# Kernel tuning notes

Hardware: AMD Instinct MI355X
Metric: run time of the kernel (lower is better)

## Reference

```python
import jax, jax.numpy as jnp
import numpy as np

BS, SEQ, NV, DM, K = 128, 2048, 64, 512, 64
MAX_ITER, TOL = 10, 1e-4


def setup_inputs() -> dict:
    key = jax.random.key(0)
    k1, k2, k3, k4 = jax.random.split(key, 4)
    x = jax.random.normal(k1, (BS, SEQ, NV), jnp.float32)
    bound = 1.0 / np.sqrt(SEQ)
    W = jax.random.uniform(k2, (DM, SEQ), jnp.float32, -bound, bound)  # nn.Linear weight
    b = jax.random.uniform(k3, (DM,), jnp.float32, -bound, bound)
    centroids = jax.random.normal(k4, (K, DM), jnp.float32)  # kaiming-uniform-init param (random stand-in)
    return {"x": x, "W": W, "b": b, "centroids": centroids}


def _kmeans(x_emb, centroids):
    # x_emb: [N, DM]; fixed-length scan with a `done` flag emulating torch's tol break.
    N = x_emb.shape[0]
    x_sq = jnp.sum(x_emb * x_emb, axis=1, keepdims=True)  # [N,1]

    def body(state, _):
        cent, ids, done = state
        # squared euclidean distances (argmin-equivalent to cdist p=2)
        d2 = x_sq - 2.0 * (x_emb @ cent.T) + jnp.sum(cent * cent, axis=1)  # [N,K]
        new_ids = jnp.argmin(d2, axis=1)
        sums = jax.ops.segment_sum(x_emb, new_ids, num_segments=K)          # [K,DM]
        counts = jax.ops.segment_sum(jnp.ones((N,), x_emb.dtype), new_ids, num_segments=K)
        means = sums / jnp.maximum(counts, 1.0)[:, None]
        new_cent = jnp.where((counts > 0)[:, None], means, cent)  # empty cluster keeps old centroid
        shift = jnp.linalg.norm(new_cent - cent)
        cent_out = jnp.where(done, cent, new_cent)
        ids_out = jnp.where(done, ids, new_ids)
        done_out = done | (shift < TOL)
        return (cent_out, ids_out, done_out), None

    init = (centroids, jnp.zeros((N,), jnp.int32), jnp.array(False))
    (cent, ids, _), _ = jax.lax.scan(body, init, None, length=MAX_ITER)
    return ids, cent


def reference(x, W, b, centroids):
    # x: [bs, seq, n_vars] -> permute -> linear(seq->d_model) -> [bs*n_vars, d_model]
    xt = jnp.transpose(x, (0, 2, 1))                 # [bs, n_vars, seq]
    x_emb = (xt @ W.T + b).reshape(-1, DM)           # [bs*n_vars, d_model]
    ids, cent = _kmeans(x_emb, centroids)
    prob = jax.nn.one_hot(ids, K, dtype=jnp.float32).reshape(BS, NV, K)
    return prob, cent, x_emb
```

## Files before the change

### kernel.cpp

```cpp
#include <hip/hip_runtime.h>

#define SEQ 2048
#define NVAR 64
#define DMODEL 512
#define BSZ 128
#define KC 64
#define NPT (BSZ*NVAR)
#define MAXIT 10

typedef __bf16 bf16x8 __attribute__((ext_vector_type(8)));
typedef float f32x4 __attribute__((ext_vector_type(4)));

__device__ __forceinline__ void load_lds16(const void* g, void* l) {
  __builtin_amdgcn_global_load_lds((const __attribute__((address_space(1))) void*)g,
                                   (__attribute__((address_space(3))) void*)l, 16, 0, 0);
}

__device__ __forceinline__ unsigned short bf16_rn(float x) {
  unsigned int u = __float_as_uint(x);
  u += 0x7fffu + ((u >> 16) & 1u);
  return (unsigned short)(u >> 16);
}

__global__ __launch_bounds__(256) void init_k(const float* __restrict__ c0,
    float* __restrict__ cent, unsigned short* __restrict__ centh,
    unsigned short* __restrict__ centl, float* __restrict__ csq4,
    int* __restrict__ done, float* __restrict__ shift2, int* __restrict__ ticket) {
  const int k = blockIdx.x, t = threadIdx.x;
  __shared__ float red[256];
  float v0, v1;
  {
    int d = t;
    v0 = c0[k * DMODEL + d];
    cent[k * DMODEL + d] = v0;
    unsigned short h = bf16_rn(v0);
    centh[k * DMODEL + d] = h;
    centl[k * DMODEL + d] = bf16_rn(v0 - __uint_as_float((unsigned)h << 16));
  }
  {
    int d = t + 256;
    v1 = c0[k * DMODEL + d];
    cent[k * DMODEL + d] = v1;
    unsigned short h = bf16_rn(v1);
    centh[k * DMODEL + d] = h;
    centl[k * DMODEL + d] = bf16_rn(v1 - __uint_as_float((unsigned)h << 16));
  }
  red[t] = v0 * v0; __syncthreads();
  for (int s = 64; s > 0; s >>= 1) { if ((t & 127) < s) red[t] += red[t + s]; __syncthreads(); }
  if (t == 0)   csq4[0 * KC + k] = red[0];
  if (t == 128) csq4[1 * KC + k] = red[128];
  __syncthreads();
  red[t] = v1 * v1; __syncthreads();
  for (int s = 64; s > 0; s >>= 1) { if ((t & 127) < s) red[t] += red[t + s]; __syncthreads(); }
  if (t == 0)   csq4[2 * KC + k] = red[0];
  if (t == 128) csq4[3 * KC + k] = red[128];
  if (k == 0 && t < MAXIT) { shift2[t] = 0.f; ticket[t] = 0; }
  if (k == 0 && t == 31) *done = 0;
}

__global__ __launch_bounds__(256) void conv_w(const float* __restrict__ W,
    unsigned short* __restrict__ Wh, unsigned short* __restrict__ Wl) {
  int i = (blockIdx.x * 256 + threadIdx.x) * 4;
  float4 v = *(const float4*)(W + i);
  ushort4 h, l;
  h.x = bf16_rn(v.x); l.x = bf16_rn(v.x - __uint_as_float((unsigned)h.x << 16));
  h.y = bf16_rn(v.y); l.y = bf16_rn(v.y - __uint_as_float((unsigned)h.y << 16));
  h.z = bf16_rn(v.z); l.z = bf16_rn(v.z - __uint_as_float((unsigned)h.z << 16));
  h.w = bf16_rn(v.w); l.w = bf16_rn(v.w - __uint_as_float((unsigned)h.w << 16));
  *(ushort4*)(Wh + i) = h;
  *(ushort4*)(Wl + i) = l;
}

__global__ __launch_bounds__(256) void conv_x(const float* __restrict__ x,
    unsigned short* __restrict__ Xh, unsigned short* __restrict__ Xl) {
  __shared__ float tile[64 * 65];
  const int k0 = blockIdx.x * 64;
  const int bs = blockIdx.y;
  const int t = threadIdx.x;
  const float* xb = x + (size_t)bs * SEQ * NVAR + (size_t)k0 * NVAR;
  #pragma unroll
  for (int p = 0; p < 4; ++p) {
    int idx = t + 256 * p;
    int row = idx >> 4, c4 = (idx & 15) * 4;
    float4 v = *(const float4*)(xb + row * NVAR + c4);
    tile[row * 65 + c4 + 0] = v.x; tile[row * 65 + c4 + 1] = v.y;
    tile[row * 65 + c4 + 2] = v.z; tile[row * 65 + c4 + 3] = v.w;
  }
  __syncthreads();
  const int v = t >> 2;
  const int kc = (t & 3) * 16;
  unsigned short h[16], l[16];
  #pragma unroll
  for (int j = 0; j < 16; ++j) {
    float f = tile[(kc + j) * 65 + v];
    h[j] = bf16_rn(f);
    l[j] = bf16_rn(f - __uint_as_float((unsigned)h[j] << 16));
  }
  size_t off = (size_t)(bs * 64 + v) * SEQ + k0 + kc;
  *(uint4*)(Xh + off)     = *(uint4*)&h[0];
  *(uint4*)(Xh + off + 8) = *(uint4*)&h[8];
  *(uint4*)(Xl + off)     = *(uint4*)&l[0];
  *(uint4*)(Xl + off + 8) = *(uint4*)&l[8];
}

__global__ __launch_bounds__(256) void gemm_mfma(
    const unsigned short* __restrict__ Ah, const unsigned short* __restrict__ Al,
    const unsigned short* __restrict__ Bh, const unsigned short* __restrict__ Bl,
    const float* __restrict__ bias, float* __restrict__ emb) {
  __shared__ unsigned short sAh[32 * 64] __attribute__((aligned(16)));
  __shared__ unsigned short sAl[32 * 64] __attribute__((aligned(16)));
  __shared__ unsigned short sBh[256 * 64] __attribute__((aligned(16)));
  __shared__ unsigned short sBl[256 * 64] __attribute__((aligned(16)));
  const int t = threadIdx.x;
  const int w = t >> 6, lane = t & 63;
  const int m0 = blockIdx.y * 32;
  const int n0 = blockIdx.x * 256;
  const int wn = w * 64;
  const int lrow = lane >> 3, sl8 = lane & 7;
  const int csrc = sl8 ^ lrow;

  f32x4 acc[2][4];
  #pragma unroll
  for (int i = 0; i < 2; ++i)
    #pragma unroll
    for (int j = 0; j < 4; ++j) acc[i][j] = (f32x4){0.f, 0.f, 0.f, 0.f};

  for (int kt = 0; kt < SEQ; kt += 64) {
    __syncthreads();
    {
      const int r = w * 8 + lrow;
      const size_t ga = (size_t)(m0 + r) * SEQ + kt + csrc * 8;
      load_lds16(Ah + ga, &sAh[r * 64 + sl8 * 8]);
      load_lds16(Al + ga, &sAl[r * 64 + sl8 * 8]);
    }
    #pragma unroll
    for (int i = 0; i < 8; ++i) {
      const int r = w * 64 + i * 8 + lrow;
      const size_t gb = (size_t)(n0 + r) * SEQ + kt + csrc * 8;
      load_lds16(Bh + gb, &sBh[r * 64 + sl8 * 8]);
      load_lds16(Bl + gb, &sBl[r * 64 + sl8 * 8]);
    }
    __syncthreads();
    #pragma unroll
    for (int kk = 0; kk < 2; ++kk) {
      const int sl = ((kk * 4 + (lane >> 4)) ^ (lane & 7)) * 8;
      bf16x8 ah[2], al[2], bh[4], bl[4];
      #pragma unroll
      for (int mi = 0; mi < 2; ++mi) {
        int off = (mi * 16 + (lane & 15)) * 64 + sl;
        ah[mi] = *(const bf16x8*)&sAh[off];
        al[mi] = *(const bf16x8*)&sAl[off];
      }
      #pragma unroll
      for (int ni = 0; ni < 4; ++ni) {
        int off = (wn + ni * 16 + (lane & 15)) * 64 + sl;
        bh[ni] = *(const bf16x8*)&sBh[off];
        bl[ni] = *(const bf16x8*)&sBl[off];
      }
      #pragma unroll
      for (int mi = 0; mi < 2; ++mi)
        #pragma unroll
        for (int ni = 0; ni < 4; ++ni) {
          acc[mi][ni] = __builtin_amdgcn_mfma_f32_16x16x32_bf16(ah[mi], bh[ni], acc[mi][ni], 0, 0, 0);
          acc[mi][ni] = __builtin_amdgcn_mfma_f32_16x16x32_bf16(ah[mi], bl[ni], acc[mi][ni], 0, 0, 0);
          acc[mi][ni] = __builtin_amdgcn_mfma_f32_16x16x32_bf16(al[mi], bh[ni], acc[mi][ni], 0, 0, 0);
        }
    }
  }
  #pragma unroll
  for (int ni = 0; ni < 4; ++ni) {
    const int n = n0 + wn + ni * 16 + (lane & 15);
    const float bv = bias[n];
    #pragma unroll
    for (int mi = 0; mi < 2; ++mi) {
      const int m = m0 + mi * 16 + (lane >> 4) * 4;
      #pragma unroll
      for (int r = 0; r < 4; ++r)
        emb[(size_t)(m + r) * DMODEL + n] = acc[mi][ni][r] + bv;
    }
  }
}

__global__ __launch_bounds__(256) void gemm_emb(const float* __restrict__ x,
    const float* __restrict__ W, const float* __restrict__ bias,
    float* __restrict__ emb) {
  __shared__ float As[64][64];
  __shared__ float Ws[64][132];
  const int bs = blockIdx.y;
  const int n0 = blockIdx.x * 128;
  const int t = threadIdx.x;
  const int tx = t & 15, ty = t >> 4;
  float bv[8];
  #pragma unroll
  for (int j = 0; j < 8; ++j) bv[j] = bias[n0 + 8 * tx + j];
  float acc[4][8];
  #pragma unroll
  for (int i = 0; i < 4; ++i)
    #pragma unroll
    for (int j = 0; j < 8; ++j) acc[i][j] = 0.f;
  const float* xb = x + (size_t)bs * SEQ * NVAR;
  for (int k0 = 0; k0 < SEQ; k0 += 64) {
    __syncthreads();
    {
      const float4* src = (const float4*)(xb + (size_t)k0 * NVAR);
      float4* dst = (float4*)&As[0][0];
      #pragma unroll
      for (int r = 0; r < 4; ++r) dst[t + 256 * r] = src[t + 256 * r];
    }
    #pragma unroll
    for (int r = 0; r < 8; ++r) {
      int idx = t + 256 * r;
      int k4 = idx & 15, n = idx >> 4;
      float4 wv = *(const float4*)(W + (size_t)(n0 + n) * SEQ + k0 + 4 * k4);
      Ws[4 * k4 + 0][n] = wv.x; Ws[4 * k4 + 1][n] = wv.y;
      Ws[4 * k4 + 2][n] = wv.z; Ws[4 * k4 + 3][n] = wv.w;
    }
    __syncthreads();
    #pragma unroll 8
    for (int kk = 0; kk < 64; ++kk) {
      const float4 a  = *(const float4*)&As[kk][4 * ty];
      const float4 w0 = *(const float4*)&Ws[kk][8 * tx];
      const float4 w1 = *(const float4*)&Ws[kk][8 * tx + 4];
      const float av[4] = {a.x, a.y, a.z, a.w};
      const float wv[8] = {w0.x, w0.y, w0.z, w0.w, w1.x, w1.y, w1.z, w1.w};
      #pragma unroll
      for (int i = 0; i < 4; ++i)
        #pragma unroll
        for (int j = 0; j < 8; ++j)
          acc[i][j] = fmaf(av[i], wv[j], acc[i][j]);
    }
  }
  #pragma unroll
  for (int i = 0; i < 4; ++i) {
    int row = bs * NVAR + 4 * ty + i;
    float4 o0 = make_float4(acc[i][0] + bv[0], acc[i][1] + bv[1],
                            acc[i][2] + bv[2], acc[i][3] + bv[3]);
    float4 o1 = make_float4(acc[i][4] + bv[4], acc[i][5] + bv[5],
                            acc[i][6] + bv[6], acc[i][7] + bv[7]);
    *(float4*)(emb + (size_t)row * DMODEL + n0 + 8 * tx) = o0;
    *(float4*)(emb + (size_t)row * DMODEL + n0 + 8 * tx + 4) = o1;
  }
}

__global__ __launch_bounds__(256) void conv_et(const float* __restrict__ emb,
    unsigned short* __restrict__ Eh, unsigned short* __restrict__ El,
    unsigned short* __restrict__ Eth, unsigned short* __restrict__ Etl) {
  __shared__ unsigned short Lh[64][72];
  __shared__ unsigned short Ll[64][72];
  const int d0 = blockIdx.x * 64;
  const int p0 = blockIdx.y * 64;
  const int t = threadIdx.x;
  #pragma unroll
  for (int q = 0; q < 2; ++q) {
    int idx = t + 256 * q;
    int r = idx >> 3, c = idx & 7;
    const float* src = emb + (size_t)(p0 + r) * DMODEL + d0 + c * 8;
    float4 v0 = *(const float4*)src;
    float4 v1 = *(const float4*)(src + 4);
    unsigned short h[8], l[8];
    const float vv[8] = {v0.x, v0.y, v0.z, v0.w, v1.x, v1.y, v1.z, v1.w};
    #pragma unroll
    for (int j = 0; j < 8; ++j) {
      h[j] = bf16_rn(vv[j]);
      l[j] = bf16_rn(vv[j] - __uint_as_float((unsigned)h[j] << 16));
    }
    size_t eo = (size_t)(p0 + r) * DMODEL + d0 + c * 8;
    *(uint4*)(Eh + eo) = *(uint4*)&h[0];
    *(uint4*)(El + eo) = *(uint4*)&l[0];
    *(uint4*)&Lh[r][c * 8] = *(uint4*)&h[0];
    *(uint4*)&Ll[r][c * 8] = *(uint4*)&l[0];
  }
  __syncthreads();
  #pragma unroll
  for (int q = 0; q < 2; ++q) {
    int idx = t + 256 * q;
    int dd = idx >> 3, pc = idx & 7;
    unsigned short h[8], l[8];
    #pragma unroll
    for (int j = 0; j < 8; ++j) {
      h[j] = Lh[pc * 8 + j][dd];
      l[j] = Ll[pc * 8 + j][dd];
    }
    size_t to = (size_t)(d0 + dd) * NPT + p0 + pc * 8;
    *(uint4*)(Eth + to) = *(uint4*)&h[0];
    *(uint4*)(Etl + to) = *(uint4*)&l[0];
  }
}

__global__ __launch_bounds__(128) void k1_assign(
    const unsigned short* __restrict__ Eh, const unsigned short* __restrict__ El,
    const unsigned short* __restrict__ Ch, const unsigned short* __restrict__ Cl,
    const float* __restrict__ csq4, const int* __restrict__ done,
    int* __restrict__ ids, float* __restrict__ pcnt) {
  if (*done) return;
  __shared__ unsigned short sEh[32 * 64] __attribute__((aligned(16)));
  __shared__ unsigned short sEl[32 * 64] __attribute__((aligned(16)));
  __shared__ unsigned short sCh[64 * 64] __attribute__((aligned(16)));
  __shared__ unsigned short sCl[64 * 64] __attribute__((aligned(16)));
  __shared__ float Dmat[32][65];
  __shared__ float csq_l[64];
  __shared__ int cnt_l[64];
  const int t = threadIdx.x;
  const int w = t >> 6, lane = t & 63;
  const int p0 = blockIdx.x * 32;
  const int lrow = lane >> 3, sl8 = lane & 7;
  const int csrc = sl8 ^ lrow;
  if (t < 64) {
    csq_l[t] = csq4[t] + csq4[KC + t] + csq4[2 * KC + t] + csq4[3 * KC + t];
    cnt_l[t] = 0;
  }

  f32x4 acc[4];
  #pragma unroll
  for (int j = 0; j < 4; ++j) acc[j] = (f32x4){0.f, 0.f, 0.f, 0.f};

  for (int kt = 0; kt < DMODEL; kt += 64) {
    __syncthreads();
    #pragma unroll
    for (int i = 0; i < 2; ++i) {
      const int r = w * 16 + i * 8 + lrow;
      const size_t ga = (size_t)(p0 + r) * DMODEL + kt + csrc * 8;
      load_lds16(Eh + ga, &sEh[r * 64 + sl8 * 8]);
      load_lds16(El + ga, &sEl[r * 64 + sl8 * 8]);
    }
    #pragma unroll
    for (int i = 0; i < 4; ++i) {
      const int r = w * 32 + i * 8 + lrow;
      const size_t gc = (size_t)r * DMODEL + kt + csrc * 8;
      load_lds16(Ch + gc, &sCh[r * 64 + sl8 * 8]);
      load_lds16(Cl + gc, &sCl[r * 64 + sl8 * 8]);
    }
    __syncthreads();
    #pragma unroll
    for (int kk = 0; kk < 2; ++kk) {
      const int sl = ((kk * 4 + (lane >> 4)) ^ (lane & 7)) * 8;
      bf16x8 eh, el, ch[4], cl[4];
      {
        int off = (w * 16 + (lane & 15)) * 64 + sl;
        eh = *(const bf16x8*)&sEh[off];
        el = *(const bf16x8*)&sEl[off];
      }
      #pragma unroll
      for (int ni = 0; ni < 4; ++ni) {
        int off = (ni * 16 + (lane & 15)) * 64 + sl;
        ch[ni] = *(const bf16x8*)&sCh[off];
        cl[ni] = *(const bf16x8*)&sCl[off];
      }
      #pragma unroll
      for (int ni = 0; ni < 4; ++ni) {
        acc[ni] = __builtin_amdgcn_mfma_f32_16x16x32_bf16(eh, ch[ni], acc[ni], 0, 0, 0);
        acc[ni] = __builtin_amdgcn_mfma_f32_16x16x32_bf16(eh, cl[ni], acc[ni], 0, 0, 0);
        acc[ni] = __builtin_amdgcn_mfma_f32_16x16x32_bf16(el, ch[ni], acc[ni], 0, 0, 0);
      }
    }
  }
  #pragma unroll
  for (int ni = 0; ni < 4; ++ni) {
    const int p = w * 16 + (lane >> 4) * 4;
    const int k = ni * 16 + (lane & 15);
    const float csq = csq_l[k];
    #pragma unroll
    for (int r = 0; r < 4; ++r)
      Dmat[p + r][k] = csq - 2.f * acc[ni][r];
  }
  __syncthreads();
  if (t < 32) {
    float best = Dmat[t][0]; int bi = 0;
    #pragma unroll 8
    for (int k = 1; k < KC; ++k) {
      float v = Dmat[t][k];
      if (v < best) { best = v; bi = k; }
    }
    ids[p0 + t] = bi;
    atomicAdd(&cnt_l[bi], 1);
  }
  __syncthreads();
  if (t < 64) pcnt[blockIdx.x * KC + t] = (float)cnt_l[t];
}

__global__ __launch_bounds__(256) void k2_segsum(
    const unsigned short* __restrict__ Eth, const unsigned short* __restrict__ Etl,
    const int* __restrict__ ids, const int* __restrict__ done,
    float* __restrict__ psum) {
  if (*done) return;
  __shared__ unsigned short sOH[64 * 136] __attribute__((aligned(16)));
  __shared__ unsigned short sTh[128 * 64] __attribute__((aligned(16)));
  __shared__ unsigned short sTl[128 * 64] __attribute__((aligned(16)));
  __shared__ int ids_l[128];
  const int t = threadIdx.x;
  const int w = t >> 6, lane = t & 63;
  const int dq = blockIdx.x, g = blockIdx.y;
  const int lrow = lane >> 3, sl8 = lane & 7;
  const int csrc = sl8 ^ lrow;

  if (t < 128) ids_l[t] = ids[g * 128 + t];
  __syncthreads();
  #pragma unroll
  for (int q = 0; q < 4; ++q) {
    int c = t * 4 + q;
    int cl = c >> 4, pc = c & 15;
    unsigned short v[8];
    #pragma unroll
    for (int j = 0; j < 8; ++j)
      v[j] = (ids_l[pc * 8 + j] == cl) ? (unsigned short)0x3F80 : (unsigned short)0;
    *(uint4*)&sOH[cl * 136 + pc * 8] = *(uint4*)&v[0];
  }

  f32x4 acc[4][2];
  #pragma unroll
  for (int i = 0; i < 4; ++i)
    #pragma unroll
    for (int j = 0; j < 2; ++j) acc[i][j] = (f32x4){0.f, 0.f, 0.f, 0.f};

  for (int kt = 0; kt < 2; ++kt) {
    __syncthreads();
    #pragma unroll
    for (int i = 0; i < 4; ++i) {
      const int rr = w * 32 + i * 8 + lrow;
      const size_t gt = (size_t)(dq * 128 + rr) * NPT + g * 128 + kt * 64 + csrc * 8;
      load_lds16(Eth + gt, &sTh[rr * 64 + sl8 * 8]);
      load_lds16(Etl + gt, &sTl[rr * 64 + sl8 * 8]);
    }
    __syncthreads();
    #pragma unroll
    for (int kk = 0; kk < 2; ++kk) {
      const int quad = lane >> 4;
      const int poff = kt * 64 + kk * 32 + quad * 8;
      bf16x8 a[4], bh[2], bl[2];
      #pragma unroll
      for (int mi = 0; mi < 4; ++mi)
        a[mi] = *(const bf16x8*)&sOH[(mi * 16 + (lane & 15)) * 136 + poff];
      const int sl = ((kk * 4 + quad) ^ (lane & 7)) * 8;
      #pragma unroll
      for (int ni = 0; ni < 2; ++ni) {
        int off = (w * 32 + ni * 16 + (lane & 15)) * 64 + sl;
        bh[ni] = *(const bf16x8*)&sTh[off];
        bl[ni] = *(const bf16x8*)&sTl[off];
      }
      #pragma unroll
      for (int mi = 0; mi < 4; ++mi)
        #pragma unroll
        for (int ni = 0; ni < 2; ++ni) {
          acc[mi][ni] = __builtin_amdgcn_mfma_f32_16x16x32_bf16(a[mi], bh[ni], acc[mi][ni], 0, 0, 0);
          acc[mi][ni] = __builtin_amdgcn_mfma_f32_16x16x32_bf16(a[mi], bl[ni], acc[mi][ni], 0, 0, 0);
        }
    }
  }
  #pragma unroll
  for (int mi = 0; mi < 4; ++mi)
    #pragma unroll
    for (int ni = 0; ni < 2; ++ni) {
      const int cl = mi * 16 + (lane >> 4) * 4;
      const int d = dq * 128 + w * 32 + ni * 16 + (lane & 15);
      #pragma unroll
      for (int r = 0; r < 4; ++r)
        psum[((size_t)g * KC + cl + r) * DMODEL + d] = acc[mi][ni][r];
    }
}

__global__ __launch_bounds__(128) void k3_update(float* __restrict__ cent,
    unsigned short* __restrict__ centh, unsigned short* __restrict__ centl,
    const float* __restrict__ psum, const float* __restrict__ pcnt,
    int* __restrict__ done, float* __restrict__ csq4,
    float* __restrict__ shift2, int* __restrict__ ticket, int iter) {
  if (*done) return;
  const int bk = blockIdx.x & 63, dq = blockIdx.x >> 6;
  const int t = threadIdx.x;
  __shared__ float red[128];
  __shared__ float cnt_s;
  red[t] = pcnt[(size_t)(2 * t) * KC + bk] + pcnt[(size_t)(2 * t + 1) * KC + bk];
  __syncthreads();
  for (int s = 64; s > 0; s >>= 1) { if (t < s) red[t] += red[t + s]; __syncthreads(); }
  if (t == 0) cnt_s = red[0];
  __syncthreads();
  const float count = cnt_s;
  const int d = dq * 128 + t;
  float s = 0.f;
  for (int g = 0; g < 64; ++g)
    s += psum[((size_t)g * KC + bk) * DMODEL + d];
  float oldv = cent[bk * DMODEL + d];
  float newv = (count > 0.f) ? (s / fmaxf(count, 1.f)) : oldv;
  cent[bk * DMODEL + d] = newv;
  unsigned short h = bf16_rn(newv);
  centh[bk * DMODEL + d] = h;
  centl[bk * DMODEL + d] = bf16_rn(newv - __uint_as_float((unsigned)h << 16));
  float df = newv - oldv;
  red[t] = df * df; __syncthreads();
  for (int s2 = 64; s2 > 0; s2 >>= 1) { if (t < s2) red[t] += red[t + s2]; __syncthreads(); }
  float tot_sh = red[0]; __syncthreads();
  red[t] = newv * newv; __syncthreads();
  for (int s2 = 64; s2 > 0; s2 >>= 1) { if (t < s2) red[t] += red[t + s2]; __syncthreads(); }
  if (t == 0) {
    csq4[dq * KC + bk] = red[0];
    atomicAdd(shift2 + iter, tot_sh);
    __threadfence();
    int tk = atomicAdd(ticket + iter, 1);
    if (tk == 255) {
      float tot = atomicAdd(shift2 + iter, 0.f);
      if (sqrtf(tot) < 1e-4f) *done = 1;
    }
  }
}

__global__ __launch_bounds__(256) void finalize_k(const int* __restrict__ ids,
    const float* __restrict__ cent, float* __restrict__ out) {
  int t = blockIdx.x * 256 + threadIdx.x;
  if (t < NPT * KC) {
    int n = t >> 6, k = t & 63;
    out[t] = (ids[n] == k) ? 1.f : 0.f;
  } else {
    int i = t - NPT * KC;
    if (i < KC * DMODEL) out[NPT * KC + i] = cent[i];
  }
}

extern "C" void kernel_launch(void* const* d_in, const int* in_sizes, int n_in,
                              void* d_out, int out_size, void* d_ws, size_t ws_size,
                              hipStream_t stream) {
  const float* x    = (const float*)d_in[0];
  const float* W    = (const float*)d_in[1];
  const float* bias = (const float*)d_in[2];
  const float* c0   = (const float*)d_in[3];
  float* out = (float*)d_out;
  float* emb_out = out + NPT * KC + KC * DMODEL;

  char* ws = (char*)d_ws;
  unsigned short* Ehi  = (unsigned short*)(ws + 0);
  unsigned short* Elo  = (unsigned short*)(ws + 8388608);
  unsigned short* Eth  = (unsigned short*)(ws + 16777216);
  unsigned short* Etl  = (unsigned short*)(ws + 25165824);
  float* psum    = (float*)(ws + 33554432);
  float* cent    = (float*)(ws + 41943040);
  unsigned short* centh = (unsigned short*)(ws + 42074112);
  unsigned short* centl = (unsigned short*)(ws + 42139648);
  float* csq4    = (float*)(ws + 42205184);
  float* shift2  = (float*)(ws + 42206208);
  int*   ticket  = (int*)(ws + 42206272);
  int*   done_f  = (int*)(ws + 42206336);
  float* pcnt    = (float*)(ws + 42206400);
  int*   ids     = (int*)(ws + 42271936);
  unsigned short* Xh = (unsigned short*)(ws + 0);
  unsigned short* Xl = (unsigned short*)(ws + 33554432);
  unsigned short* Wh = (unsigned short*)(ws + 67108864);
  unsigned short* Wl = (unsigned short*)(ws + 69206016);
  const size_t need_fast = 71303168;
  (void)n_in; (void)in_sizes; (void)out_size;

  if (ws_size >= need_fast) {
    conv_w<<<1024, 256, 0, stream>>>(W, Wh, Wl);
    conv_x<<<dim3(32, BSZ), 256, 0, stream>>>(x, Xh, Xl);
    gemm_mfma<<<dim3(2, 256), 256, 0, stream>>>(Xh, Xl, Wh, Wl, bias, emb_out);
  } else {
    gemm_emb<<<dim3(4, BSZ), 256, 0, stream>>>(x, W, bias, emb_out);
  }
  init_k<<<KC, 256, 0, stream>>>(c0, cent, centh, centl, csq4, done_f, shift2, ticket);
  conv_et<<<dim3(8, 128), 256, 0, stream>>>(emb_out, Ehi, Elo, Eth, Etl);
  for (int it = 0; it < MAXIT; ++it) {
    k1_assign<<<256, 128, 0, stream>>>(Ehi, Elo, centh, centl, csq4, done_f, ids, pcnt);
    k2_segsum<<<dim3(4, 64), 256, 0, stream>>>(Eth, Etl, ids, done_f, psum);
    k3_update<<<256, 128, 0, stream>>>(cent, centh, centl, psum, pcnt, done_f,
                                       csq4, shift2, ticket, it);
  }
  finalize_k<<<2176, 256, 0, stream>>>(ids, cent, out);
}
```

Before: 477.5 us.

## Fuse k-means assignment and segment-sum kernels into one per-iteration kernel

Merges the distance/argmin kernel and the one-hot segment-sum kernel into a single kernel. Each block assigns 128 points using a shuffle-based argmin and keeps the ids in shared memory, then immediately builds the one-hot matrix for its d-slice. This removes one launch per iteration and the global round trip of ids. The cost is that the assignment GEMM is recomputed by each of the four d-slice blocks. The embedding GEMM grid is also transposed so consecutive blocks walk M instead of N, changing cache reuse of the inputs.

```diff
diff --git a/kernel.cpp b/kernel.cpp
--- a/kernel.cpp
+++ b/kernel.cpp
@@ -113,8 +113,8 @@
   __shared__ unsigned short sBl[256 * 64] __attribute__((aligned(16)));
   const int t = threadIdx.x;
   const int w = t >> 6, lane = t & 63;
-  const int m0 = blockIdx.y * 32;
-  const int n0 = blockIdx.x * 256;
+  const int m0 = blockIdx.x * 32;
+  const int n0 = blockIdx.y * 256;
   const int wn = w * 64;
   const int lrow = lane >> 3, sl8 = lane & 7;
   const int csrc = sl8 ^ lrow;
@@ -287,175 +287,180 @@
   }
 }
 
-__global__ __launch_bounds__(128) void k1_assign(
+__global__ __launch_bounds__(256) void k12_fused(
     const unsigned short* __restrict__ Eh, const unsigned short* __restrict__ El,
+    const unsigned short* __restrict__ Eth, const unsigned short* __restrict__ Etl,
     const unsigned short* __restrict__ Ch, const unsigned short* __restrict__ Cl,
     const float* __restrict__ csq4, const int* __restrict__ done,
-    int* __restrict__ ids, float* __restrict__ pcnt) {
+    int* __restrict__ ids, float* __restrict__ pcnt, float* __restrict__ psum) {
   if (*done) return;
-  __shared__ unsigned short sEh[32 * 64] __attribute__((aligned(16)));
-  __shared__ unsigned short sEl[32 * 64] __attribute__((aligned(16)));
-  __shared__ unsigned short sCh[64 * 64] __attribute__((aligned(16)));
-  __shared__ unsigned short sCl[64 * 64] __attribute__((aligned(16)));
-  __shared__ float Dmat[32][65];
+  __shared__ __align__(16) unsigned char smem[50176];
   __shared__ float csq_l[64];
   __shared__ int cnt_l[64];
-  const int t = threadIdx.x;
-  const int w = t >> 6, lane = t & 63;
-  const int p0 = blockIdx.x * 32;
-  const int lrow = lane >> 3, sl8 = lane & 7;
-  const int csrc = sl8 ^ lrow;
-  if (t < 64) {
-    csq_l[t] = csq4[t] + csq4[KC + t] + csq4[2 * KC + t] + csq4[3 * KC + t];
-    cnt_l[t] = 0;
-  }
-
-  f32x4 acc[4];
-  #pragma unroll
-  for (int j = 0; j < 4; ++j) acc[j] = (f32x4){0.f, 0.f, 0.f, 0.f};
-
-  for (int kt = 0; kt < DMODEL; kt += 64) {
-    __syncthreads();
-    #pragma unroll
-    for (int i = 0; i < 2; ++i) {
-      const int r = w * 16 + i * 8 + lrow;
-      const size_t ga = (size_t)(p0 + r) * DMODEL + kt + csrc * 8;
-      load_lds16(Eh + ga, &sEh[r * 64 + sl8 * 8]);
-      load_lds16(El + ga, &sEl[r * 64 + sl8 * 8]);
-    }
-    #pragma unroll
-    for (int i = 0; i < 4; ++i) {
-      const int r = w * 32 + i * 8 + lrow;
-      const size_t gc = (size_t)r * DMODEL + kt + csrc * 8;
-      load_lds16(Ch + gc, &sCh[r * 64 + sl8 * 8]);
-      load_lds16(Cl + gc, &sCl[r * 64 + sl8 * 8]);
-    }
-    __syncthreads();
-    #pragma unroll
-    for (int kk = 0; kk < 2; ++kk) {
-      const int sl = ((kk * 4 + (lane >> 4)) ^ (lane & 7)) * 8;
-      bf16x8 eh, el, ch[4], cl[4];
-      {
-        int off = (w * 16 + (lane & 15)) * 64 + sl;
-        eh = *(const bf16x8*)&sEh[off];
-        el = *(const bf16x8*)&sEl[off];
-      }
-      #pragma unroll
-      for (int ni = 0; ni < 4; ++ni) {
-        int off = (ni * 16 + (lane & 15)) * 64 + sl;
-        ch[ni] = *(const bf16x8*)&sCh[off];
-        cl[ni] = *(const bf16x8*)&sCl[off];
-      }
-      #pragma unroll
-      for (int ni = 0; ni < 4; ++ni) {
-        acc[ni] = __builtin_amdgcn_mfma_f32_16x16x32_bf16(eh, ch[ni], acc[ni], 0, 0, 0);
-        acc[ni] = __builtin_amdgcn_mfma_f32_16x16x32_bf16(eh, cl[ni], acc[ni], 0, 0, 0);
-        acc[ni] = __builtin_amdgcn_mfma_f32_16x16x32_bf16(el, ch[ni], acc[ni], 0, 0, 0);
-      }
-    }
-  }
-  #pragma unroll
-  for (int ni = 0; ni < 4; ++ni) {
-    const int p = w * 16 + (lane >> 4) * 4;
-    const int k = ni * 16 + (lane & 15);
-    const float csq = csq_l[k];
-    #pragma unroll
-    for (int r = 0; r < 4; ++r)
-      Dmat[p + r][k] = csq - 2.f * acc[ni][r];
-  }
-  __syncthreads();
-  if (t < 32) {
-    float best = Dmat[t][0]; int bi = 0;
-    #pragma unroll 8
-    for (int k = 1; k < KC; ++k) {
-      float v = Dmat[t][k];
-      if (v < best) { best = v; bi = k; }
-    }
-    ids[p0 + t] = bi;
-    atomicAdd(&cnt_l[bi], 1);
-  }
-  __syncthreads();
-  if (t < 64) pcnt[blockIdx.x * KC + t] = (float)cnt_l[t];
-}
-
-__global__ __launch_bounds__(256) void k2_segsum(
-    const unsigned short* __restrict__ Eth, const unsigned short* __restrict__ Etl,
-    const int* __restrict__ ids, const int* __restrict__ done,
-    float* __restrict__ psum) {
-  if (*done) return;
-  __shared__ unsigned short sOH[64 * 136] __attribute__((aligned(16)));
-  __shared__ unsigned short sTh[128 * 64] __attribute__((aligned(16)));
-  __shared__ unsigned short sTl[128 * 64] __attribute__((aligned(16)));
   __shared__ int ids_l[128];
   const int t = threadIdx.x;
   const int w = t >> 6, lane = t & 63;
-  const int dq = blockIdx.x, g = blockIdx.y;
+  const int g = blockIdx.x & 63, dq = blockIdx.x >> 6;
+  const int p0 = g * 128;
   const int lrow = lane >> 3, sl8 = lane & 7;
   const int csrc = sl8 ^ lrow;
 
-  if (t < 128) ids_l[t] = ids[g * 128 + t];
+  {
+    unsigned short* sEh = (unsigned short*)smem;
+    unsigned short* sEl = (unsigned short*)(smem + 16384);
+    unsigned short* sCh = (unsigned short*)(smem + 32768);
+    unsigned short* sCl = (unsigned short*)(smem + 40960);
+    if (t < 64) {
+      csq_l[t] = csq4[t] + csq4[KC + t] + csq4[2 * KC + t] + csq4[3 * KC + t];
+      cnt_l[t] = 0;
+    }
+    f32x4 acc[2][4];
+    #pragma unroll
+    for (int i = 0; i < 2; ++i)
+      #pragma unroll
+      for (int j = 0; j < 4; ++j) acc[i][j] = (f32x4){0.f, 0.f, 0.f, 0.f};
+
+    for (int kt = 0; kt < DMODEL; kt += 64) {
+      __syncthreads();
+      #pragma unroll
+      for (int i = 0; i < 4; ++i) {
+        const int r = w * 32 + i * 8 + lrow;
+        const size_t ga = (size_t)(p0 + r) * DMODEL + kt + csrc * 8;
+        load_lds16(Eh + ga, &sEh[r * 64 + sl8 * 8]);
+        load_lds16(El + ga, &sEl[r * 64 + sl8 * 8]);
+      }
+      #pragma unroll
+      for (int i = 0; i < 2; ++i) {
+        const int r = w * 16 + i * 8 + lrow;
+        const size_t gc = (size_t)r * DMODEL + kt + csrc * 8;
+        load_lds16(Ch + gc, &sCh[r * 64 + sl8 * 8]);
+        load_lds16(Cl + gc, &sCl[r * 64 + sl8 * 8]);
+      }
+      __syncthreads();
+      #pragma unroll
+      for (int kk = 0; kk < 2; ++kk) {
+        const int sl = ((kk * 4 + (lane >> 4)) ^ (lane & 7)) * 8;
+        bf16x8 eh[2], el[2], ch[4], cl[4];
+        #pragma unroll
+        for (int mi = 0; mi < 2; ++mi) {
+          int off = (w * 32 + mi * 16 + (lane & 15)) * 64 + sl;
+          eh[mi] = *(const bf16x8*)&sEh[off];
+          el[mi] = *(const bf16x8*)&sEl[off];
+        }
+        #pragma unroll
+        for (int ni = 0; ni < 4; ++ni) {
+          int off = (ni * 16 + (lane & 15)) * 64 + sl;
+          ch[ni] = *(const bf16x8*)&sCh[off];
+          cl[ni] = *(const bf16x8*)&sCl[off];
+        }
+        #pragma unroll
+        for (int mi = 0; mi < 2; ++mi)
+          #pragma unroll
+          for (int ni = 0; ni < 4; ++ni) {
+            acc[mi][ni] = __builtin_amdgcn_mfma_f32_16x16x32_bf16(eh[mi], ch[ni], acc[mi][ni], 0, 0, 0);
+            acc[mi][ni] = __builtin_amdgcn_mfma_f32_16x16x32_bf16(eh[mi], cl[ni], acc[mi][ni], 0, 0, 0);
+            acc[mi][ni] = __builtin_amdgcn_mfma_f32_16x16x32_bf16(el[mi], ch[ni], acc[mi][ni], 0, 0, 0);
+          }
+      }
+    }
+    #pragma unroll
+    for (int mi = 0; mi < 2; ++mi) {
+      #pragma unroll
+      for (int r = 0; r < 4; ++r) {
+        float bv = csq_l[lane & 15] - 2.f * acc[mi][0][r];
+        int bk = lane & 15;
+        #pragma unroll
+        for (int ni = 1; ni < 4; ++ni) {
+          const int k = ni * 16 + (lane & 15);
+          float v = csq_l[k] - 2.f * acc[mi][ni][r];
+          if (v < bv) { bv = v; bk = k; }
+        }
+        #pragma unroll
+        for (int m = 1; m < 16; m <<= 1) {
+          float ov = __shfl_xor(bv, m, 64);
+          int   ok = __shfl_xor(bk, m, 64);
+          if (ov < bv || (ov == bv && ok < bk)) { bv = ov; bk = ok; }
+        }
+        if ((lane & 15) == 0) {
+          const int p = w * 32 + mi * 16 + (lane >> 4) * 4 + r;
+          ids_l[p] = bk;
+          atomicAdd(&cnt_l[bk], 1);
+        }
+      }
+    }
+  }
   __syncthreads();
-  #pragma unroll
-  for (int q = 0; q < 4; ++q) {
-    int c = t * 4 + q;
-    int cl = c >> 4, pc = c & 15;
-    unsigned short v[8];
-    #pragma unroll
-    for (int j = 0; j < 8; ++j)
-      v[j] = (ids_l[pc * 8 + j] == cl) ? (unsigned short)0x3F80 : (unsigned short)0;
-    *(uint4*)&sOH[cl * 136 + pc * 8] = *(uint4*)&v[0];
-  }
-
-  f32x4 acc[4][2];
-  #pragma unroll
-  for (int i = 0; i < 4; ++i)
-    #pragma unroll
-    for (int j = 0; j < 2; ++j) acc[i][j] = (f32x4){0.f, 0.f, 0.f, 0.f};
-
-  for (int kt = 0; kt < 2; ++kt) {
-    __syncthreads();
-    #pragma unroll
-    for (int i = 0; i < 4; ++i) {
-      const int rr = w * 32 + i * 8 + lrow;
-      const size_t gt = (size_t)(dq * 128 + rr) * NPT + g * 128 + kt * 64 + csrc * 8;
-      load_lds16(Eth + gt, &sTh[rr * 64 + sl8 * 8]);
-      load_lds16(Etl + gt, &sTl[rr * 64 + sl8 * 8]);
-    }
-    __syncthreads();
-    #pragma unroll
-    for (int kk = 0; kk < 2; ++kk) {
-      const int quad = lane >> 4;
-      const int poff = kt * 64 + kk * 32 + quad * 8;
-      bf16x8 a[4], bh[2], bl[2];
-      #pragma unroll
-      for (int mi = 0; mi < 4; ++mi)
-        a[mi] = *(const bf16x8*)&sOH[(mi * 16 + (lane & 15)) * 136 + poff];
-      const int sl = ((kk * 4 + quad) ^ (lane & 7)) * 8;
+  if (dq == 0) {
+    if (t < 128) ids[p0 + t] = ids_l[t];
+    if (t < 64) pcnt[g * KC + t] = (float)cnt_l[t];
+  }
+
+  {
+    unsigned short* sOH = (unsigned short*)smem;
+    unsigned short* sTh = (unsigned short*)(smem + 17408);
+    unsigned short* sTl = (unsigned short*)(smem + 33792);
+    #pragma unroll
+    for (int q = 0; q < 4; ++q) {
+      int c = t * 4 + q;
+      int cl = c >> 4, pc = c & 15;
+      unsigned short v[8];
+      #pragma unroll
+      for (int j = 0; j < 8; ++j)
+        v[j] = (ids_l[pc * 8 + j] == cl) ? (unsigned short)0x3F80 : (unsigned short)0;
+      *(uint4*)&sOH[cl * 136 + pc * 8] = *(uint4*)&v[0];
+    }
+
+    f32x4 acc[4][2];
+    #pragma unroll
+    for (int i = 0; i < 4; ++i)
+      #pragma unroll
+      for (int j = 0; j < 2; ++j) acc[i][j] = (f32x4){0.f, 0.f, 0.f, 0.f};
+
+    for (int kt = 0; kt < 2; ++kt) {
+      __syncthreads();
+      #pragma unroll
+      for (int i = 0; i < 4; ++i) {
+        const int rr = w * 32 + i * 8 + lrow;
+        const size_t gt = (size_t)(dq * 128 + rr) * NPT + g * 128 + kt * 64 + csrc * 8;
+        load_lds16(Eth + gt, &sTh[rr * 64 + sl8 * 8]);
+        load_lds16(Etl + gt, &sTl[rr * 64 + sl8 * 8]);
+      }
+      __syncthreads();
+      #pragma unroll
+      for (int kk = 0; kk < 2; ++kk) {
+        const int quad = lane >> 4;
+        const int poff = kt * 64 + kk * 32 + quad * 8;
+        bf16x8 a[4], bh[2], bl[2];
+        #pragma unroll
+        for (int mi = 0; mi < 4; ++mi)
+          a[mi] = *(const bf16x8*)&sOH[(mi * 16 + (lane & 15)) * 136 + poff];
+        const int sl = ((kk * 4 + quad) ^ (lane & 7)) * 8;
+        #pragma unroll
+        for (int ni = 0; ni < 2; ++ni) {
+          int off = (w * 32 + ni * 16 + (lane & 15)) * 64 + sl;
+          bh[ni] = *(const bf16x8*)&sTh[off];
+          bl[ni] = *(const bf16x8*)&sTl[off];
+        }
+        #pragma unroll
+        for (int mi = 0; mi < 4; ++mi)
+          #pragma unroll
+          for (int ni = 0; ni < 2; ++ni) {
+            acc[mi][ni] = __builtin_amdgcn_mfma_f32_16x16x32_bf16(a[mi], bh[ni], acc[mi][ni], 0, 0, 0);
+            acc[mi][ni] = __builtin_amdgcn_mfma_f32_16x16x32_bf16(a[mi], bl[ni], acc[mi][ni], 0, 0, 0);
+          }
+      }
+    }
+    #pragma unroll
+    for (int mi = 0; mi < 4; ++mi)
       #pragma unroll
       for (int ni = 0; ni < 2; ++ni) {
-        int off = (w * 32 + ni * 16 + (lane & 15)) * 64 + sl;
-        bh[ni] = *(const bf16x8*)&sTh[off];
-        bl[ni] = *(const bf16x8*)&sTl[off];
-      }
-      #pragma unroll
-      for (int mi = 0; mi < 4; ++mi)
-        #pragma unroll
-        for (int ni = 0; ni < 2; ++ni) {
-          acc[mi][ni] = __builtin_amdgcn_mfma_f32_16x16x32_bf16(a[mi], bh[ni], acc[mi][ni], 0, 0, 0);
-          acc[mi][ni] = __builtin_amdgcn_mfma_f32_16x16x32_bf16(a[mi], bl[ni], acc[mi][ni], 0, 0, 0);
-        }
-    }
-  }
-  #pragma unroll
-  for (int mi = 0; mi < 4; ++mi)
-    #pragma unroll
-    for (int ni = 0; ni < 2; ++ni) {
-      const int cl = mi * 16 + (lane >> 4) * 4;
-      const int d = dq * 128 + w * 32 + ni * 16 + (lane & 15);
-      #pragma unroll
-      for (int r = 0; r < 4; ++r)
-        psum[((size_t)g * KC + cl + r) * DMODEL + d] = acc[mi][ni][r];
-    }
+        const int cl = mi * 16 + (lane >> 4) * 4;
+        const int d = dq * 128 + w * 32 + ni * 16 + (lane & 15);
+        #pragma unroll
+        for (int r = 0; r < 4; ++r)
+          psum[((size_t)g * KC + cl + r) * DMODEL + d] = acc[mi][ni][r];
+      }
+  }
 }
 
 __global__ __launch_bounds__(128) void k3_update(float* __restrict__ cent,
@@ -468,7 +473,7 @@
   const int t = threadIdx.x;
   __shared__ float red[128];
   __shared__ float cnt_s;
-  red[t] = pcnt[(size_t)(2 * t) * KC + bk] + pcnt[(size_t)(2 * t + 1) * KC + bk];
+  red[t] = (t < 64) ? pcnt[(size_t)t * KC + bk] : 0.f;
   __syncthreads();
   for (int s = 64; s > 0; s >>= 1) { if (t < s) red[t] += red[t + s]; __syncthreads(); }
   if (t == 0) cnt_s = red[0];
@@ -549,15 +554,15 @@
   if (ws_size >= need_fast) {
     conv_w<<<1024, 256, 0, stream>>>(W, Wh, Wl);
     conv_x<<<dim3(32, BSZ), 256, 0, stream>>>(x, Xh, Xl);
-    gemm_mfma<<<dim3(2, 256), 256, 0, stream>>>(Xh, Xl, Wh, Wl, bias, emb_out);
+    gemm_mfma<<<dim3(256, 2), 256, 0, stream>>>(Xh, Xl, Wh, Wl, bias, emb_out);
   } else {
     gemm_emb<<<dim3(4, BSZ), 256, 0, stream>>>(x, W, bias, emb_out);
   }
   init_k<<<KC, 256, 0, stream>>>(c0, cent, centh, centl, csq4, done_f, shift2, ticket);
   conv_et<<<dim3(8, 128), 256, 0, stream>>>(emb_out, Ehi, Elo, Eth, Etl);
   for (int it = 0; it < MAXIT; ++it) {
-    k1_assign<<<256, 128, 0, stream>>>(Ehi, Elo, centh, centl, csq4, done_f, ids, pcnt);
-    k2_segsum<<<dim3(4, 64), 256, 0, stream>>>(Eth, Etl, ids, done_f, psum);
+    k12_fused<<<256, 256, 0, stream>>>(Ehi, Elo, Eth, Etl, centh, centl,
+                                       csq4, done_f, ids, pcnt, psum);
     k3_update<<<256, 128, 0, stream>>>(cent, centh, centl, psum, pcnt, done_f,
                                        csq4, shift2, ticket, it);
   }
```

After: 506.0 us. 1.06x slower.
